# Kernel optimization log

Measured on AMD Instinct MI355X. Metric: run time of the kernel, lower is better.

The kernel has to match this reference:

```python
import jax, jax.numpy as jnp
import numpy as np

N_NODES = 100000
N_EDGES = 1600000
IN_CH = 128
OUT_CH = 64
NEG_SLOPE = 0.2
EPS = 1e-10


def setup_inputs() -> dict:
    key = jax.random.key(0)
    k1, k2, k3, k4, k5 = jax.random.split(key, 5)
    x = jax.random.normal(k1, (N_NODES, IN_CH), dtype=jnp.float32)
    edge_index = jax.random.randint(k2, (2, N_EDGES), 0, N_NODES, dtype=jnp.int64)
    W = jax.random.normal(k3, (OUT_CH, IN_CH), dtype=jnp.float32) * (1.0 / np.sqrt(IN_CH))
    a_l = jax.random.normal(k4, (OUT_CH,), dtype=jnp.float32) * (1.0 / np.sqrt(OUT_CH))
    a_r = jax.random.normal(k5, (OUT_CH,), dtype=jnp.float32) * (1.0 / np.sqrt(OUT_CH))
    bias = jnp.zeros((OUT_CH,), dtype=jnp.float32)
    return {"x": x, "edge_index": edge_index, "W": W, "a_l": a_l, "a_r": a_r, "bias": bias}


def reference(x, edge_index, W, a_l, a_r, bias):
    N = x.shape[0]
    h = x @ W.T                     # (N, out_ch)
    src, dst = edge_index[0], edge_index[1]
    e_l = h @ a_l                   # (N,)
    e_r = h @ a_r                   # (N,)
    edge_attn = jax.nn.leaky_relu(e_l[dst] + e_r[src], negative_slope=NEG_SLOPE)  # (E,)
    # segment softmax over incoming edges of each dst node
    edge_max = jax.ops.segment_max(edge_attn, dst, num_segments=N)  # (N,), -inf for isolated
    edge_attn = jnp.exp(edge_attn - edge_max[dst])
    edge_sum = jax.ops.segment_sum(edge_attn, dst, num_segments=N)  # (N,)
    edge_attn = edge_attn / (edge_sum[dst] + EPS)
    messages = h[src] * edge_attn[:, None]                          # (E, out_ch)
    out = jax.ops.segment_sum(messages, dst, num_segments=N)        # (N, out_ch)
    return out + bias
```

## Files before the change

kernel.cpp:

```cpp
#include <hip/hip_runtime.h>
#include <math.h>

#define NN 100000
#define NE 1600000
#define IC 128
#define OC 64
#define NEG_SLOPE 0.2f
#define EPS_F 1e-10f

#define NSLICE 200
#define SN 500
#define EB 500
#define QPB 800
#define CAP 12000

typedef short bf16x8 __attribute__((ext_vector_type(8)));
typedef float f32x4 __attribute__((ext_vector_type(4)));

__device__ __forceinline__ unsigned short f2bf(float f) {
    unsigned u = __float_as_uint(f);
    u += 0x7fff + ((u >> 16) & 1);
    return (unsigned short)(u >> 16);
}

__global__ __launch_bounds__(256) void linear_kernel(
    const float* __restrict__ x, const float* __restrict__ W,
    const float* __restrict__ a_l, const float* __restrict__ a_r,
    unsigned short* __restrict__ h_bf, float* __restrict__ e_l,
    float* __restrict__ e_r)
{
    __shared__ unsigned short lds[128 * 136];
    const int tid = threadIdx.x;
    const int n0 = blockIdx.x * 64;

#pragma unroll
    for (int it = 0; it < 8; it++) {
        int i = it * 256 + tid;
        int r = i >> 5, c4 = i & 31;
        int n = n0 + r;
        float4 v = make_float4(0.f, 0.f, 0.f, 0.f);
        if (n < NN) v = *(const float4*)&x[(size_t)n * 128 + (c4 << 2)];
        ushort4 b;
        b.x = f2bf(v.x); b.y = f2bf(v.y); b.z = f2bf(v.z); b.w = f2bf(v.w);
        *(ushort4*)&lds[r * 136 + (c4 << 2)] = b;
    }
#pragma unroll
    for (int it = 0; it < 8; it++) {
        int i = it * 256 + tid;
        int r = i >> 5, c4 = i & 31;
        float4 v = *(const float4*)&W[r * 128 + (c4 << 2)];
        ushort4 b;
        b.x = f2bf(v.x); b.y = f2bf(v.y); b.z = f2bf(v.z); b.w = f2bf(v.w);
        *(ushort4*)&lds[(64 + r) * 136 + (c4 << 2)] = b;
    }
    __syncthreads();

    const int wv = tid >> 6;
    const int lane = tid & 63;
    const int q = lane >> 4;
    const int c = lane & 15;

    f32x4 acc[4];
#pragma unroll
    for (int t = 0; t < 4; t++) acc[t] = (f32x4){0.f, 0.f, 0.f, 0.f};

    const unsigned short* xrow = &lds[(wv * 16 + c) * 136];
    const unsigned short* wrow = &lds[(64 + c) * 136];

#pragma unroll
    for (int kk = 0; kk < 4; kk++) {
        int ko = kk * 32 + q * 8;
        bf16x8 a = *(const bf16x8*)&xrow[ko];
#pragma unroll
        for (int t = 0; t < 4; t++) {
            bf16x8 b = *(const bf16x8*)&wrow[t * 16 * 136 + ko];
            acc[t] = __builtin_amdgcn_mfma_f32_16x16x32_bf16(a, b, acc[t], 0, 0, 0);
        }
    }

#pragma unroll
    for (int r = 0; r < 4; r++) {
        int m = n0 + wv * 16 + q * 4 + r;
        if (m < NN) {
#pragma unroll
            for (int t = 0; t < 4; t++)
                h_bf[(size_t)m * OC + t * 16 + c] = f2bf(acc[t][r]);
        }
    }

    float al[4], ar[4];
#pragma unroll
    for (int t = 0; t < 4; t++) { al[t] = a_l[t * 16 + c]; ar[t] = a_r[t * 16 + c]; }
    float pl[4], pr[4];
#pragma unroll
    for (int r = 0; r < 4; r++) {
        pl[r] = al[0] * acc[0][r] + al[1] * acc[1][r] + al[2] * acc[2][r] + al[3] * acc[3][r];
        pr[r] = ar[0] * acc[0][r] + ar[1] * acc[1][r] + ar[2] * acc[2][r] + ar[3] * acc[3][r];
    }
#pragma unroll
    for (int m = 1; m < 16; m <<= 1) {
#pragma unroll
        for (int r = 0; r < 4; r++) {
            pl[r] += __shfl_xor(pl[r], m);
            pr[r] += __shfl_xor(pr[r], m);
        }
    }
    if (c == 0) {
#pragma unroll
        for (int r = 0; r < 4; r++) {
            int m = n0 + wv * 16 + q * 4 + r;
            if (m < NN) { e_l[m] = pl[r]; e_r[m] = pr[r]; }
        }
    }
}

__global__ __launch_bounds__(256) void hist_kernel(
    const int* __restrict__ dst, int* __restrict__ H)
{
    __shared__ int hist[NSLICE];
    const int t = threadIdx.x, b = blockIdx.x;
    if (t < NSLICE) hist[t] = 0;
    __syncthreads();
    for (int qi = t; qi < QPB; qi += 256) {
        int4 d = ((const int4*)dst)[b * QPB + qi];
        atomicAdd(&hist[d.x / SN], 1);
        atomicAdd(&hist[d.y / SN], 1);
        atomicAdd(&hist[d.z / SN], 1);
        atomicAdd(&hist[d.w / SN], 1);
    }
    __syncthreads();
    if (t < NSLICE) H[t * EB + b] = hist[t];
}

__global__ __launch_bounds__(1024) void scan_block_kernel(
    const int* __restrict__ deg, int* __restrict__ offsets,
    int* __restrict__ bsums)
{
    __shared__ int wsum[16];
    const int t = threadIdx.x;
    const int lane = t & 63, wv = t >> 6;
    const int i = blockIdx.x * 1024 + t;
    int v = (i < NN) ? deg[i] : 0;
    int incl = v;
#pragma unroll
    for (int off = 1; off < 64; off <<= 1) {
        int u = __shfl_up(incl, off);
        if (lane >= off) incl += u;
    }
    if (lane == 63) wsum[wv] = incl;
    __syncthreads();
    if (wv == 0 && lane < 16) {
        int s = wsum[lane];
        int si = s;
#pragma unroll
        for (int off = 1; off < 16; off <<= 1) {
            int u = __shfl_up(si, off);
            if (lane >= off) si += u;
        }
        wsum[lane] = si - s;
    }
    __syncthreads();
    int excl = incl - v + wsum[wv];
    if (i < NN) offsets[i] = excl;
    if (t == 1023) bsums[blockIdx.x] = excl + v;
}

__global__ __launch_bounds__(128) void scan_bsums_kernel(
    int* __restrict__ bsums, int* __restrict__ offsets)
{
    __shared__ int s[128];
    const int t = threadIdx.x;
    const int NB = (NN + 1023) / 1024;
    int v = (t < NB) ? bsums[t] : 0;
    s[t] = v;
    __syncthreads();
    for (int off = 1; off < 128; off <<= 1) {
        int u = (t >= off) ? s[t - off] : 0;
        __syncthreads();
        s[t] += u;
        __syncthreads();
    }
    if (t < NB) bsums[t] = s[t] - v;
    if (t == NB - 1) offsets[NN] = s[t];
}

__global__ __launch_bounds__(1024) void scan_add_kernel(
    int* __restrict__ offsets, const int* __restrict__ bsums)
{
    int i = blockIdx.x * 1024 + threadIdx.x;
    if (i < NN) offsets[i] += bsums[blockIdx.x];
}

__global__ __launch_bounds__(256) void bucket_kernel(
    const int* __restrict__ src, const int* __restrict__ dst,
    const int* __restrict__ O_flat, int* __restrict__ bucketed)
{
    __shared__ int cur[NSLICE];
    const int t = threadIdx.x, b = blockIdx.x;
    if (t < NSLICE) cur[t] = O_flat[t * EB + b];
    __syncthreads();
    for (int qi = t; qi < QPB; qi += 256) {
        int4 d4 = ((const int4*)dst)[b * QPB + qi];
        int4 s4 = ((const int4*)src)[b * QPB + qi];
        int dd[4] = {d4.x, d4.y, d4.z, d4.w};
        int ss[4] = {s4.x, s4.y, s4.z, s4.w};
#pragma unroll
        for (int k = 0; k < 4; k++) {
            int sl = dd[k] / SN;
            int pos = atomicAdd(&cur[sl], 1);
            bucketed[pos] = ((dd[k] - sl * SN) << 17) | ss[k];
        }
    }
}

__global__ __launch_bounds__(1024) void fine_sort_kernel(
    const int* __restrict__ bucketed, const int* __restrict__ O_flat,
    int* __restrict__ sorted_src, int* __restrict__ offsets_out)
{
    __shared__ int ebuf[CAP];
    __shared__ int hist[SN];
    __shared__ int wsums[8];
    const int s = blockIdx.x, t = threadIdx.x;
    const int B0 = O_flat[s * EB];
    int cnt = O_flat[(s + 1) * EB] - B0;
    if (cnt > CAP) cnt = CAP;

    for (int i = t; i < cnt; i += 1024) ebuf[i] = bucketed[B0 + i];
    for (int i = t; i < SN; i += 1024) hist[i] = 0;
    __syncthreads();
    for (int i = t; i < cnt; i += 1024) atomicAdd(&hist[ebuf[i] >> 17], 1);
    __syncthreads();

    const int lane = t & 63, w = t >> 6;
    int v = (t < SN) ? hist[t] : 0;
    int incl = v;
#pragma unroll
    for (int o = 1; o < 64; o <<= 1) {
        int u = __shfl_up(incl, o);
        if (lane >= o) incl += u;
    }
    if (w < 8 && lane == 63) wsums[w] = incl;
    __syncthreads();
    if (t == 0) {
        int run = 0;
#pragma unroll
        for (int k = 0; k < 8; k++) { int x = wsums[k]; wsums[k] = run; run += x; }
    }
    __syncthreads();
    int excl = incl - v + ((w < 8) ? wsums[w] : 0);

    if (t < SN) offsets_out[s * SN + t] = B0 + excl;
    __syncthreads();
    if (t < SN) hist[t] = excl;
    __syncthreads();
    for (int i = t; i < cnt; i += 1024) {
        int p = ebuf[i];
        int pos = atomicAdd(&hist[p >> 17], 1);
        sorted_src[B0 + pos] = p & 0x1FFFF;
    }
    if (s == 0 && t == 0) offsets_out[NN] = NE;
}

__global__ __launch_bounds__(256) void aggregate_kernel(
    const unsigned short* __restrict__ h_bf, const int* __restrict__ offsets,
    const int* __restrict__ sorted_src, const float* __restrict__ e_l,
    const float* __restrict__ e_r, const float* __restrict__ bias,
    float* __restrict__ out)
{
    const int node = blockIdx.x * 4 + (threadIdx.x >> 6);
    const int lane = threadIdx.x & 63;
    if (node >= NN) return;
    const int start = offsets[node];
    const int end = offsets[node + 1];
    const int grp = lane >> 3;
    const int ch = (lane & 7) * 8;
    const float el = e_l[node];

    float acc[8] = {0.f, 0.f, 0.f, 0.f, 0.f, 0.f, 0.f, 0.f};
    float wsum = 0.f;

#pragma unroll 2
    for (int j = start; j < end; j += 8) {
        int eidx = j + grp;
        int ej = (eidx < end) ? eidx : end - 1;
        int s = sorted_src[ej];
        float a = el + e_r[s];
        a = (a > 0.f) ? a : NEG_SLOPE * a;
        float w = (eidx < end) ? __expf(a) : 0.f;
        uint4 qv = *(const uint4*)&h_bf[(size_t)s * OC + ch];
        wsum += w;
        acc[0] += w * __uint_as_float(qv.x << 16);
        acc[1] += w * __uint_as_float(qv.x & 0xffff0000u);
        acc[2] += w * __uint_as_float(qv.y << 16);
        acc[3] += w * __uint_as_float(qv.y & 0xffff0000u);
        acc[4] += w * __uint_as_float(qv.z << 16);
        acc[5] += w * __uint_as_float(qv.z & 0xffff0000u);
        acc[6] += w * __uint_as_float(qv.w << 16);
        acc[7] += w * __uint_as_float(qv.w & 0xffff0000u);
    }

#pragma unroll
    for (int m = 8; m <= 32; m <<= 1) {
#pragma unroll
        for (int k = 0; k < 8; k++) acc[k] += __shfl_xor(acc[k], m);
        wsum += __shfl_xor(wsum, m);
    }

    if (lane < 8) {
        float inv = 1.f / (wsum + EPS_F);
        float4 b0 = *(const float4*)&bias[lane * 8];
        float4 b1 = *(const float4*)&bias[lane * 8 + 4];
        float4 o0 = make_float4(acc[0] * inv + b0.x, acc[1] * inv + b0.y,
                                acc[2] * inv + b0.z, acc[3] * inv + b0.w);
        float4 o1 = make_float4(acc[4] * inv + b1.x, acc[5] * inv + b1.y,
                                acc[6] * inv + b1.z, acc[7] * inv + b1.w);
        *(float4*)&out[(size_t)node * OC + lane * 8] = o0;
        *(float4*)&out[(size_t)node * OC + lane * 8 + 4] = o1;
    }
}

extern "C" void kernel_launch(void* const* d_in, const int* in_sizes, int n_in,
                              void* d_out, int out_size, void* d_ws, size_t ws_size,
                              hipStream_t stream)
{
    const float* x = (const float*)d_in[0];
    const int* edge_index = (const int*)d_in[1];
    const float* W = (const float*)d_in[2];
    const float* a_l = (const float*)d_in[3];
    const float* a_r = (const float*)d_in[4];
    const float* bias = (const float*)d_in[5];
    float* out = (float*)d_out;

    const int* src = edge_index;
    const int* dst = edge_index + NE;

    char* w = (char*)d_ws;
    unsigned short* h_bf = (unsigned short*)w;
    size_t off = (size_t)NN * OC * 2;
    float* e_l = (float*)(w + off); off += (size_t)NN * 4;
    float* e_r = (float*)(w + off); off += (size_t)NN * 4;
    int* H = (int*)(w + off);       off += (size_t)NN * 4;
    int* O_flat = (int*)(w + off);  off += (size_t)(NN + 4) * 4;
    int* bsums = (int*)(w + off);   off += 128 * 4;
    int* offsets = (int*)(w + off); off += (size_t)(NN + 4) * 4;
    int* bucketed = (int*)(w + off); off += (size_t)NE * 4;
    int* sorted_src = (int*)(w + off); off += (size_t)NE * 4;

    linear_kernel<<<(NN + 63) / 64, 256, 0, stream>>>(x, W, a_l, a_r, h_bf, e_l, e_r);
    hist_kernel<<<EB, 256, 0, stream>>>(dst, H);
    scan_block_kernel<<<(NN + 1023) / 1024, 1024, 0, stream>>>(H, O_flat, bsums);
    scan_bsums_kernel<<<1, 128, 0, stream>>>(bsums, O_flat);
    scan_add_kernel<<<(NN + 1023) / 1024, 1024, 0, stream>>>(O_flat, bsums);
    bucket_kernel<<<EB, 256, 0, stream>>>(src, dst, O_flat, bucketed);
    fine_sort_kernel<<<NSLICE, 1024, 0, stream>>>(bucketed, O_flat, sorted_src, offsets);
    aggregate_kernel<<<(NN + 3) / 4, 256, 0, stream>>>(h_bf, offsets, sorted_src,
                                                       e_l, e_r, bias, out);
}
```

Baseline: 202.7 us.

## Fold scan-add into consumers and precompute normalized attention weights in fine sort

Removes the scan_add kernel by having bucket and fine_sort add the block prefix sums on the fly. Moves the per-edge attention exp and softmax normalization into fine_sort, which uses shared-memory float atomics for the per-destination sums and writes (src, weight) pairs. Aggregation then only gathers h rows scaled by the precomputed weight, with no e_r gather, exp or wsum reduction. In exchange, the sorted edge array doubles in size, fine_sort needs more shared memory (an extra CAP-sized float buffer), and shared float atomics make summation order nondeterministic.

```diff
diff --git a/kernel.cpp b/kernel.cpp
--- a/kernel.cpp
+++ b/kernel.cpp
@@ -165,8 +165,7 @@
     if (t == 1023) bsums[blockIdx.x] = excl + v;
 }
 
-__global__ __launch_bounds__(128) void scan_bsums_kernel(
-    int* __restrict__ bsums, int* __restrict__ offsets)
+__global__ __launch_bounds__(128) void scan_bsums_kernel(int* __restrict__ bsums)
 {
     __shared__ int s[128];
     const int t = threadIdx.x;
@@ -181,23 +180,19 @@
         __syncthreads();
     }
     if (t < NB) bsums[t] = s[t] - v;
-    if (t == NB - 1) offsets[NN] = s[t];
-}
-
-__global__ __launch_bounds__(1024) void scan_add_kernel(
-    int* __restrict__ offsets, const int* __restrict__ bsums)
-{
-    int i = blockIdx.x * 1024 + threadIdx.x;
-    if (i < NN) offsets[i] += bsums[blockIdx.x];
 }
 
 __global__ __launch_bounds__(256) void bucket_kernel(
     const int* __restrict__ src, const int* __restrict__ dst,
-    const int* __restrict__ O_flat, int* __restrict__ bucketed)
+    const int* __restrict__ O_raw, const int* __restrict__ bsums,
+    int* __restrict__ bucketed)
 {
     __shared__ int cur[NSLICE];
     const int t = threadIdx.x, b = blockIdx.x;
-    if (t < NSLICE) cur[t] = O_flat[t * EB + b];
+    if (t < NSLICE) {
+        int gi = t * EB + b;
+        cur[t] = O_raw[gi] + bsums[gi >> 10];
+    }
     __syncthreads();
     for (int qi = t; qi < QPB; qi += 256) {
         int4 d4 = ((const int4*)dst)[b * QPB + qi];
@@ -214,24 +209,49 @@
 }
 
 __global__ __launch_bounds__(1024) void fine_sort_kernel(
-    const int* __restrict__ bucketed, const int* __restrict__ O_flat,
-    int* __restrict__ sorted_src, int* __restrict__ offsets_out)
+    const int* __restrict__ bucketed, const int* __restrict__ O_raw,
+    const int* __restrict__ bsums, const float* __restrict__ e_l,
+    const float* __restrict__ e_r, float2* __restrict__ sorted_sw,
+    int* __restrict__ offsets_out)
 {
     __shared__ int ebuf[CAP];
+    __shared__ float wbuf[CAP];
     __shared__ int hist[SN];
+    __shared__ float nsum[SN];
+    __shared__ float el[SN];
     __shared__ int wsums[8];
     const int s = blockIdx.x, t = threadIdx.x;
-    const int B0 = O_flat[s * EB];
-    int cnt = O_flat[(s + 1) * EB] - B0;
+    int gi0 = s * EB;
+    const int B0 = O_raw[gi0] + bsums[gi0 >> 10];
+    int B1 = NE;
+    if (s < NSLICE - 1) {
+        int gi1 = (s + 1) * EB;
+        B1 = O_raw[gi1] + bsums[gi1 >> 10];
+    }
+    int cnt = B1 - B0;
     if (cnt > CAP) cnt = CAP;
 
     for (int i = t; i < cnt; i += 1024) ebuf[i] = bucketed[B0 + i];
-    for (int i = t; i < SN; i += 1024) hist[i] = 0;
-    __syncthreads();
-    for (int i = t; i < cnt; i += 1024) atomicAdd(&hist[ebuf[i] >> 17], 1);
-    __syncthreads();
-
-    const int lane = t & 63, w = t >> 6;
+    if (t < SN) {
+        hist[t] = 0;
+        nsum[t] = 0.f;
+        el[t] = e_l[s * SN + t];
+    }
+    __syncthreads();
+    for (int i = t; i < cnt; i += 1024) {
+        int p = ebuf[i];
+        int dloc = p >> 17;
+        int sr = p & 0x1FFFF;
+        float a = el[dloc] + e_r[sr];
+        a = (a > 0.f) ? a : NEG_SLOPE * a;
+        float w = __expf(a);
+        wbuf[i] = w;
+        atomicAdd(&hist[dloc], 1);
+        atomicAdd(&nsum[dloc], w);
+    }
+    __syncthreads();
+
+    const int lane = t & 63, w8 = t >> 6;
     int v = (t < SN) ? hist[t] : 0;
     int incl = v;
 #pragma unroll
@@ -239,7 +259,7 @@
         int u = __shfl_up(incl, o);
         if (lane >= o) incl += u;
     }
-    if (w < 8 && lane == 63) wsums[w] = incl;
+    if (w8 < 8 && lane == 63) wsums[w8] = incl;
     __syncthreads();
     if (t == 0) {
         int run = 0;
@@ -247,7 +267,7 @@
         for (int k = 0; k < 8; k++) { int x = wsums[k]; wsums[k] = run; run += x; }
     }
     __syncthreads();
-    int excl = incl - v + ((w < 8) ? wsums[w] : 0);
+    int excl = incl - v + ((w8 < 8) ? wsums[w8] : 0);
 
     if (t < SN) offsets_out[s * SN + t] = B0 + excl;
     __syncthreads();
@@ -255,16 +275,17 @@
     __syncthreads();
     for (int i = t; i < cnt; i += 1024) {
         int p = ebuf[i];
-        int pos = atomicAdd(&hist[p >> 17], 1);
-        sorted_src[B0 + pos] = p & 0x1FFFF;
+        int dloc = p >> 17;
+        int pos = atomicAdd(&hist[dloc], 1);
+        float wn = wbuf[i] / (nsum[dloc] + EPS_F);
+        sorted_sw[B0 + pos] = make_float2(__int_as_float(p & 0x1FFFF), wn);
     }
     if (s == 0 && t == 0) offsets_out[NN] = NE;
 }
 
 __global__ __launch_bounds__(256) void aggregate_kernel(
     const unsigned short* __restrict__ h_bf, const int* __restrict__ offsets,
-    const int* __restrict__ sorted_src, const float* __restrict__ e_l,
-    const float* __restrict__ e_r, const float* __restrict__ bias,
+    const float2* __restrict__ sorted_sw, const float* __restrict__ bias,
     float* __restrict__ out)
 {
     const int node = blockIdx.x * 4 + (threadIdx.x >> 6);
@@ -274,21 +295,17 @@
     const int end = offsets[node + 1];
     const int grp = lane >> 3;
     const int ch = (lane & 7) * 8;
-    const float el = e_l[node];
 
     float acc[8] = {0.f, 0.f, 0.f, 0.f, 0.f, 0.f, 0.f, 0.f};
-    float wsum = 0.f;
 
 #pragma unroll 2
     for (int j = start; j < end; j += 8) {
         int eidx = j + grp;
         int ej = (eidx < end) ? eidx : end - 1;
-        int s = sorted_src[ej];
-        float a = el + e_r[s];
-        a = (a > 0.f) ? a : NEG_SLOPE * a;
-        float w = (eidx < end) ? __expf(a) : 0.f;
+        float2 p = sorted_sw[ej];
+        float w = (eidx < end) ? p.y : 0.f;
+        int s = __float_as_int(p.x);
         uint4 qv = *(const uint4*)&h_bf[(size_t)s * OC + ch];
-        wsum += w;
         acc[0] += w * __uint_as_float(qv.x << 16);
         acc[1] += w * __uint_as_float(qv.x & 0xffff0000u);
         acc[2] += w * __uint_as_float(qv.y << 16);
@@ -303,17 +320,15 @@
     for (int m = 8; m <= 32; m <<= 1) {
 #pragma unroll
         for (int k = 0; k < 8; k++) acc[k] += __shfl_xor(acc[k], m);
-        wsum += __shfl_xor(wsum, m);
     }
 
     if (lane < 8) {
-        float inv = 1.f / (wsum + EPS_F);
         float4 b0 = *(const float4*)&bias[lane * 8];
         float4 b1 = *(const float4*)&bias[lane * 8 + 4];
-        float4 o0 = make_float4(acc[0] * inv + b0.x, acc[1] * inv + b0.y,
-                                acc[2] * inv + b0.z, acc[3] * inv + b0.w);
-        float4 o1 = make_float4(acc[4] * inv + b1.x, acc[5] * inv + b1.y,
-                                acc[6] * inv + b1.z, acc[7] * inv + b1.w);
+        float4 o0 = make_float4(acc[0] + b0.x, acc[1] + b0.y,
+                                acc[2] + b0.z, acc[3] + b0.w);
+        float4 o1 = make_float4(acc[4] + b1.x, acc[5] + b1.y,
+                                acc[6] + b1.z, acc[7] + b1.w);
         *(float4*)&out[(size_t)node * OC + lane * 8] = o0;
         *(float4*)&out[(size_t)node * OC + lane * 8 + 4] = o1;
     }
@@ -340,19 +355,18 @@
     float* e_l = (float*)(w + off); off += (size_t)NN * 4;
     float* e_r = (float*)(w + off); off += (size_t)NN * 4;
     int* H = (int*)(w + off);       off += (size_t)NN * 4;
-    int* O_flat = (int*)(w + off);  off += (size_t)(NN + 4) * 4;
+    int* O_raw = (int*)(w + off);   off += (size_t)(NN + 4) * 4;
     int* bsums = (int*)(w + off);   off += 128 * 4;
     int* offsets = (int*)(w + off); off += (size_t)(NN + 4) * 4;
     int* bucketed = (int*)(w + off); off += (size_t)NE * 4;
-    int* sorted_src = (int*)(w + off); off += (size_t)NE * 4;
+    float2* sorted_sw = (float2*)(w + off); off += (size_t)NE * 8;
 
     linear_kernel<<<(NN + 63) / 64, 256, 0, stream>>>(x, W, a_l, a_r, h_bf, e_l, e_r);
     hist_kernel<<<EB, 256, 0, stream>>>(dst, H);
-    scan_block_kernel<<<(NN + 1023) / 1024, 1024, 0, stream>>>(H, O_flat, bsums);
-    scan_bsums_kernel<<<1, 128, 0, stream>>>(bsums, O_flat);
-    scan_add_kernel<<<(NN + 1023) / 1024, 1024, 0, stream>>>(O_flat, bsums);
-    bucket_kernel<<<EB, 256, 0, stream>>>(src, dst, O_flat, bucketed);
-    fine_sort_kernel<<<NSLICE, 1024, 0, stream>>>(bucketed, O_flat, sorted_src, offsets);
-    aggregate_kernel<<<(NN + 3) / 4, 256, 0, stream>>>(h_bf, offsets, sorted_src,
-                                                       e_l, e_r, bias, out);
-}
+    scan_block_kernel<<<(NN + 1023) / 1024, 1024, 0, stream>>>(H, O_raw, bsums);
+    scan_bsums_kernel<<<1, 128, 0, stream>>>(bsums);
+    bucket_kernel<<<EB, 256, 0, stream>>>(src, dst, O_raw, bsums, bucketed);
+    fine_sort_kernel<<<NSLICE, 1024, 0, stream>>>(bucketed, O_raw, bsums, e_l, e_r,
+                                                  sorted_sw, offsets);
+    aggregate_kernel<<<(NN + 3) / 4, 256, 0, stream>>>(h_bf, offsets, sorted_sw, bias, out);
+}
```

Measured after the change: 199.1 us. Within noise of the previous version (-1.8%).
